# Kernel tuning notes

Hardware: AMD Instinct MI355X
Metric: run time of the kernel (lower is better)

## Reference

```python
import jax, jax.numpy as jnp
from jax import lax
import numpy as np

D_MODEL, D_STATE, EXPAND, D_CONV = 1024, 16, 2, 4
D_INNER = EXPAND * D_MODEL
B, L = 4, 2048


def setup_inputs() -> dict:
    key = jax.random.key(0)
    ks = jax.random.split(key, 12)
    def xavier(k, shape):
        fan_in, fan_out = shape[1], shape[0]
        lim = float(np.sqrt(6.0 / (fan_in + fan_out)))
        return jax.random.uniform(k, shape, jnp.float32, -lim, lim)
    inp = {}
    inp['x'] = jax.random.normal(ks[0], (B, L, D_MODEL), jnp.float32)
    inp['W_left'] = xavier(ks[1], (D_INNER, D_MODEL))
    inp['conv_w'] = jax.random.normal(ks[2], (D_INNER, 1, D_CONV), jnp.float32) * (1.0 / np.sqrt(D_CONV))
    inp['conv_b'] = jax.random.normal(ks[3], (D_INNER,), jnp.float32) * 0.01
    inp['W_delta'] = jax.random.normal(ks[4], (D_INNER, D_INNER), jnp.float32) * (1.0 / np.sqrt(D_INNER))
    inp['b_delta'] = jnp.zeros((D_INNER,), jnp.float32)
    inp['W_B'] = jax.random.normal(ks[5], (D_STATE, D_INNER), jnp.float32) * (1.0 / np.sqrt(D_INNER))
    inp['W_C'] = jax.random.normal(ks[6], (D_STATE, D_INNER), jnp.float32) * (1.0 / np.sqrt(D_INNER))
    inp['A_log'] = jnp.log(jnp.arange(1, D_STATE + 1, dtype=jnp.float32))
    inp['W_right'] = xavier(ks[7], (D_INNER, D_MODEL))
    inp['ln_g'] = jnp.ones((D_INNER,), jnp.float32)
    inp['ln_b'] = jnp.zeros((D_INNER,), jnp.float32)
    inp['W_out'] = xavier(ks[8], (D_MODEL, D_INNER))
    return inp


def _ssm(xl, W_delta, b_delta, W_B, W_C, A_log):
    # xl: [b, l, d_inner]
    b, l, d_inner = xl.shape
    A = -jax.nn.softplus(A_log)  # [d_state]
    delta = jnp.clip(jax.nn.softplus(xl @ W_delta.T + b_delta), 1e-4, 10.0)
    Bm = xl @ W_B.T  # [b, l, d_state]
    Cm = xl @ W_C.T  # [b, l, d_state]

    def step(h, inp):
        d_t, x_t, B_t, C_t = inp  # [b,d_inner], [b,d_inner], [b,N], [b,N]
        A_bar = jnp.exp(d_t[:, :, None] * A)            # [b, d_inner, N]
        h = A_bar * h + (d_t * x_t)[:, :, None] * B_t[:, None, :]
        y_t = jnp.einsum('bdn,bn->bd', h, C_t)
        return h, y_t

    h0 = jnp.zeros((b, d_inner, A_log.shape[0]), xl.dtype)
    xs = (jnp.swapaxes(delta, 0, 1), jnp.swapaxes(xl, 0, 1),
          jnp.swapaxes(Bm, 0, 1), jnp.swapaxes(Cm, 0, 1))
    _, ys = lax.scan(step, h0, xs)  # ys: [l, b, d_inner]
    return jnp.swapaxes(ys, 0, 1)


def reference(x, W_left, conv_w, conv_b, W_delta, b_delta, W_B, W_C, A_log,
              W_right, ln_g, ln_b, W_out):
    d_conv = conv_w.shape[-1]
    # left branch: linear -> causal depthwise conv1d -> silu
    left = x @ W_left.T                          # [b, l, d_inner]
    left_ncw = jnp.swapaxes(left, 1, 2)          # [b, d_inner, l]
    left_ncw = jnp.pad(left_ncw, ((0, 0), (0, 0), (d_conv - 1, 0)))
    left_ncw = lax.conv_general_dilated(
        left_ncw, conv_w, window_strides=(1,), padding='VALID',
        feature_group_count=conv_w.shape[0]) + conv_b[None, :, None]
    left = jax.nn.silu(jnp.swapaxes(left_ncw, 1, 2))
    # selective scan
    ssm_out = _ssm(left, W_delta, b_delta, W_B, W_C, A_log)
    # right gate (eval mode: dropout off)
    gate = jax.nn.silu(x @ W_right.T)
    out = ssm_out * gate
    # layernorm over d_inner
    mu = jnp.mean(out, axis=-1, keepdims=True)
    var = jnp.mean(jnp.square(out - mu), axis=-1, keepdims=True)
    out = (out - mu) * lax.rsqrt(var + 1e-5) * ln_g + ln_b
    return out @ W_out.T
```

## Files before the change

kernel.cpp:

```cpp
#include <hip/hip_runtime.h>
#include <cstddef>

#define LL 2048
#define TOK 8192
#define DM 1024
#define DI 2048
#define NS 16

typedef _Float16 half_t;
typedef __attribute__((ext_vector_type(8))) _Float16 f16x8;
typedef __attribute__((ext_vector_type(4))) _Float16 f16x4;
typedef __attribute__((ext_vector_type(4))) float f32x4;

__device__ __forceinline__ float softplus_f(float x) {
  return fmaxf(x, 0.f) + log1pf(__expf(-fabsf(x)));
}
__device__ __forceinline__ float silu_f(float x) {
  return x / (1.f + __expf(-x));
}
__device__ __forceinline__ void gload_lds16(const void* g, void* l) {
  __builtin_amdgcn_global_load_lds((const __attribute__((address_space(1))) void*)g,
                                   (__attribute__((address_space(3))) void*)l, 16, 0, 0);
}
#define DPP_ADD(v, ctrl) \
  ((v) + __int_as_float(__builtin_amdgcn_update_dpp(0, __float_as_int(v), (ctrl), 0xf, 0xf, true)))

__device__ float g_buf[120881152];

__global__ __launch_bounds__(256) void f2h_k(const float* __restrict__ in,
                                             half_t* __restrict__ out, int n4) {
  const int i = blockIdx.x * 256 + threadIdx.x;
  if (i >= n4) return;
  const float4 v = ((const float4*)in)[i];
  f16x4 o;
  o[0] = (half_t)v.x; o[1] = (half_t)v.y; o[2] = (half_t)v.z; o[3] = (half_t)v.w;
  ((f16x4*)out)[i] = o;
}

__global__ __launch_bounds__(256) void f2h2_k(const float* __restrict__ in,
                                              half_t* __restrict__ hi,
                                              half_t* __restrict__ lo, int n4) {
  const int i = blockIdx.x * 256 + threadIdx.x;
  if (i >= n4) return;
  const float4 v = ((const float4*)in)[i];
  f16x4 h, l;
  h[0] = (half_t)v.x; h[1] = (half_t)v.y; h[2] = (half_t)v.z; h[3] = (half_t)v.w;
  l[0] = (half_t)(v.x - (float)h[0]);
  l[1] = (half_t)(v.y - (float)h[1]);
  l[2] = (half_t)(v.z - (float)h[2]);
  l[3] = (half_t)(v.w - (float)h[3]);
  ((f16x4*)hi)[i] = h;
  ((f16x4*)lo)[i] = l;
}

template <int ACT>
__global__ __launch_bounds__(256) void gemm_mfma(const half_t* __restrict__ A,
                                                 const half_t* __restrict__ W,
                                                 const float* __restrict__ bias,
                                                 float* __restrict__ C,
                                                 int M, int N, int K) {
  __shared__ half_t lA[4096];
  __shared__ half_t lB[4096];
  const int tid = threadIdx.x;
  const int bm0 = blockIdx.y * 128, bn0 = blockIdx.x * 128;
  const int lane = tid & 63, wave = tid >> 6;
  const int q = lane >> 4, mr = lane & 15;
  const int wm = (wave >> 1) * 64, wn = (wave & 1) * 64;
  const int flat0 = tid, flat1 = tid + 256;
  const int kc0 = flat0 >> 7, r0 = flat0 & 127;
  const int kc1 = flat1 >> 7, r1 = flat1 & 127;

  f32x4 acc[4][4];
#pragma unroll
  for (int i = 0; i < 4; ++i)
#pragma unroll
    for (int j = 0; j < 4; ++j) acc[i][j] = (f32x4){0.f, 0.f, 0.f, 0.f};

  for (int k0 = 0; k0 < K; k0 += 32) {
    gload_lds16(A + (size_t)(bm0 + r0) * K + k0 + kc0 * 8, lA + (size_t)flat0 * 8);
    gload_lds16(A + (size_t)(bm0 + r1) * K + k0 + kc1 * 8, lA + (size_t)flat1 * 8);
    gload_lds16(W + (size_t)(bn0 + r0) * K + k0 + kc0 * 8, lB + (size_t)flat0 * 8);
    gload_lds16(W + (size_t)(bn0 + r1) * K + k0 + kc1 * 8, lB + (size_t)flat1 * 8);
    __syncthreads();
    f16x8 af[4], bg[4];
#pragma unroll
    for (int t = 0; t < 4; ++t) {
      af[t] = *(const f16x8*)(lA + ((q << 10) + ((wm + t * 16 + mr) << 3)));
      bg[t] = *(const f16x8*)(lB + ((q << 10) + ((wn + t * 16 + mr) << 3)));
    }
#pragma unroll
    for (int i = 0; i < 4; ++i)
#pragma unroll
      for (int j = 0; j < 4; ++j)
        acc[i][j] = __builtin_amdgcn_mfma_f32_16x16x32_f16(af[i], bg[j], acc[i][j], 0, 0, 0);
    __syncthreads();
  }

#pragma unroll
  for (int i = 0; i < 4; ++i) {
#pragma unroll
    for (int j = 0; j < 4; ++j) {
      const int col = bn0 + wn + j * 16 + mr;
      const float bv = bias ? bias[col] : 0.f;
#pragma unroll
      for (int r = 0; r < 4; ++r) {
        const int row = bm0 + wm + i * 16 + q * 4 + r;
        float v = acc[i][j][r] + bv;
        if (ACT == 1) v = silu_f(v);
        C[(size_t)row * N + col] = v;
      }
    }
  }
}

__global__ __launch_bounds__(256) void gemm_mfma_lg(const half_t* __restrict__ A,
                                                    const half_t* __restrict__ W,
                                                    float* __restrict__ left,
                                                    float* __restrict__ gate) {
  __shared__ half_t lA[4096];
  __shared__ half_t lB[4096];
  const int tid = threadIdx.x;
  const int bm0 = blockIdx.y * 128, bn0 = blockIdx.x * 128;
  const int K = DM;
  const int lane = tid & 63, wave = tid >> 6;
  const int q = lane >> 4, mr = lane & 15;
  const int wm = (wave >> 1) * 64, wn = (wave & 1) * 64;
  const int flat1 = tid + 256;
  const int kc0 = tid >> 7, r0 = tid & 127;
  const int kc1 = flat1 >> 7, r1 = flat1 & 127;

  f32x4 acc[4][4];
#pragma unroll
  for (int i = 0; i < 4; ++i)
#pragma unroll
    for (int j = 0; j < 4; ++j) acc[i][j] = (f32x4){0.f, 0.f, 0.f, 0.f};

  for (int k0 = 0; k0 < K; k0 += 32) {
    gload_lds16(A + (size_t)(bm0 + r0) * K + k0 + kc0 * 8, lA + (size_t)tid * 8);
    gload_lds16(A + (size_t)(bm0 + r1) * K + k0 + kc1 * 8, lA + (size_t)flat1 * 8);
    gload_lds16(W + (size_t)(bn0 + r0) * K + k0 + kc0 * 8, lB + (size_t)tid * 8);
    gload_lds16(W + (size_t)(bn0 + r1) * K + k0 + kc1 * 8, lB + (size_t)flat1 * 8);
    __syncthreads();
    f16x8 af[4], bg[4];
#pragma unroll
    for (int t = 0; t < 4; ++t) {
      af[t] = *(const f16x8*)(lA + ((q << 10) + ((wm + t * 16 + mr) << 3)));
      bg[t] = *(const f16x8*)(lB + ((q << 10) + ((wn + t * 16 + mr) << 3)));
    }
#pragma unroll
    for (int i = 0; i < 4; ++i)
#pragma unroll
      for (int j = 0; j < 4; ++j)
        acc[i][j] = __builtin_amdgcn_mfma_f32_16x16x32_f16(af[i], bg[j], acc[i][j], 0, 0, 0);
    __syncthreads();
  }

  const int is_gate = (bn0 >= DI);
  float* out = is_gate ? gate : left;
  const int cb = bn0 - (is_gate ? DI : 0);
#pragma unroll
  for (int i = 0; i < 4; ++i) {
#pragma unroll
    for (int j = 0; j < 4; ++j) {
      const int col = cb + wn + j * 16 + mr;
#pragma unroll
      for (int r = 0; r < 4; ++r) {
        const int row = bm0 + wm + i * 16 + q * 4 + r;
        float v = acc[i][j][r];
        if (is_gate) v = silu_f(v);
        out[(size_t)row * DI + col] = v;
      }
    }
  }
}

__global__ __launch_bounds__(512, 4) void gemm_mfma_split(const half_t* __restrict__ Ah,
                                                          const half_t* __restrict__ Wh,
                                                          const half_t* __restrict__ Wl,
                                                          const float* __restrict__ bias,
                                                          float* __restrict__ C,
                                                          int M, int N, int K) {
  __shared__ half_t lAh[8192];
  __shared__ half_t lBh[4096], lBl[4096];
  const int tid = threadIdx.x;
  const int bm0 = blockIdx.y * 256, bn0 = blockIdx.x * 128;
  const int lane = tid & 63, wave = tid >> 6;
  const int q = lane >> 4, mr = lane & 15;
  const int wm = (wave >> 1) * 64, wn = (wave & 1) * 64;
  const int aflat1 = tid + 512;
  const int akc0 = tid >> 8, ar0 = tid & 255;
  const int akc1 = aflat1 >> 8, ar1 = aflat1 & 255;
  const int wkc = tid >> 7, wr = tid & 127;

  f32x4 acc[4][4];
#pragma unroll
  for (int i = 0; i < 4; ++i)
#pragma unroll
    for (int j = 0; j < 4; ++j) acc[i][j] = (f32x4){0.f, 0.f, 0.f, 0.f};

  for (int k0 = 0; k0 < K; k0 += 32) {
    gload_lds16(Ah + (size_t)(bm0 + ar0) * K + k0 + akc0 * 8, lAh + (size_t)tid * 8);
    gload_lds16(Ah + (size_t)(bm0 + ar1) * K + k0 + akc1 * 8, lAh + (size_t)aflat1 * 8);
    gload_lds16(Wh + (size_t)(bn0 + wr) * K + k0 + wkc * 8, lBh + (size_t)tid * 8);
    gload_lds16(Wl + (size_t)(bn0 + wr) * K + k0 + wkc * 8, lBl + (size_t)tid * 8);
    __syncthreads();
    f16x8 ah[4], bh[4], bl[4];
#pragma unroll
    for (int t = 0; t < 4; ++t) {
      const int ao = (q << 11) + ((wm + t * 16 + mr) << 3);
      const int bo = (q << 10) + ((wn + t * 16 + mr) << 3);
      ah[t] = *(const f16x8*)(lAh + ao);
      bh[t] = *(const f16x8*)(lBh + bo);
      bl[t] = *(const f16x8*)(lBl + bo);
    }
#pragma unroll
    for (int i = 0; i < 4; ++i)
#pragma unroll
      for (int j = 0; j < 4; ++j) {
        acc[i][j] = __builtin_amdgcn_mfma_f32_16x16x32_f16(ah[i], bh[j], acc[i][j], 0, 0, 0);
        acc[i][j] = __builtin_amdgcn_mfma_f32_16x16x32_f16(ah[i], bl[j], acc[i][j], 0, 0, 0);
      }
    __syncthreads();
  }

  const int wmg = (wave >> 1) * 64;
#pragma unroll
  for (int i = 0; i < 4; ++i) {
#pragma unroll
    for (int j = 0; j < 4; ++j) {
      const int col = bn0 + wn + j * 16 + mr;
      const float bv = bias[col];
#pragma unroll
      for (int r = 0; r < 4; ++r) {
        const int row = bm0 + wmg + i * 16 + q * 4 + r;
        float v = softplus_f(acc[i][j][r] + bv);
        v = fminf(fmaxf(v, 1e-4f), 10.f);
        C[(size_t)row * N + col] = v;
      }
    }
  }
}

__global__ __launch_bounds__(256) void bc_mfma(const half_t* __restrict__ A,
                                               const half_t* __restrict__ Wbc,
                                               float* __restrict__ bc) {
  __shared__ half_t lA[4096];
  __shared__ half_t lB[1024];
  const int tid = threadIdx.x;
  const int bm0 = blockIdx.x * 128;
  const int lane = tid & 63, wave = tid >> 6;
  const int q = lane >> 4, mr = lane & 15;
  const int wm = wave * 32;
  const int flat1 = tid + 256;
  const int kcA0 = tid >> 7, rA0 = tid & 127;
  const int kcA1 = flat1 >> 7, rA1 = flat1 & 127;
  const int kcB = tid >> 5, rB = tid & 31;

  f32x4 acc[2][2];
#pragma unroll
  for (int i = 0; i < 2; ++i)
#pragma unroll
    for (int j = 0; j < 2; ++j) acc[i][j] = (f32x4){0.f, 0.f, 0.f, 0.f};

  for (int k0 = 0; k0 < DI; k0 += 32) {
    gload_lds16(A + (size_t)(bm0 + rA0) * DI + k0 + kcA0 * 8, lA + (size_t)tid * 8);
    gload_lds16(A + (size_t)(bm0 + rA1) * DI + k0 + kcA1 * 8, lA + (size_t)flat1 * 8);
    if (tid < 128)
      gload_lds16(Wbc + (size_t)rB * DI + k0 + kcB * 8, lB + (size_t)tid * 8);
    __syncthreads();
    f16x8 af[2], bg[2];
#pragma unroll
    for (int t = 0; t < 2; ++t) {
      af[t] = *(const f16x8*)(lA + ((q << 10) + ((wm + t * 16 + mr) << 3)));
      bg[t] = *(const f16x8*)(lB + ((q << 8) + ((t * 16 + mr) << 3)));
    }
#pragma unroll
    for (int i = 0; i < 2; ++i)
#pragma unroll
      for (int j = 0; j < 2; ++j)
        acc[i][j] = __builtin_amdgcn_mfma_f32_16x16x32_f16(af[i], bg[j], acc[i][j], 0, 0, 0);
    __syncthreads();
  }

#pragma unroll
  for (int i = 0; i < 2; ++i) {
#pragma unroll
    for (int j = 0; j < 2; ++j) {
#pragma unroll
      for (int r = 0; r < 4; ++r) {
        const int row = bm0 + wm + i * 16 + q * 4 + r;
        bc[(size_t)row * 32 + 2 * mr + j] = acc[i][j][r];
      }
    }
  }
}

__global__ __launch_bounds__(256) void conv_silu_k(const float* __restrict__ left,
                                                   const float* __restrict__ cw,
                                                   const float* __restrict__ cb,
                                                   float* __restrict__ xc,
                                                   half_t* __restrict__ xch) {
  const int idx = blockIdx.x * 256 + threadIdx.x;
  const int d = idx & (DI - 1);
  const int bt = idx >> 11;
  const int t = bt & (LL - 1);
  const float4 wv = *(const float4*)(cw + (size_t)d * 4);
  float acc = cb[d];
  const size_t base = (size_t)idx;
  if (t >= 3) {
    acc += left[base - 3 * DI] * wv.x + left[base - 2 * DI] * wv.y +
           left[base - DI] * wv.z + left[base] * wv.w;
  } else {
    acc += left[base] * wv.w;
    if (t >= 1) acc += left[base - DI] * wv.z;
    if (t >= 2) acc += left[base - 2 * DI] * wv.y;
  }
  const float v = silu_f(acc);
  xc[base] = v;
  xch[base] = (half_t)v;
}

#define ST 32
__global__ __launch_bounds__(256) void scan_k(const float* __restrict__ delta,
                                              const float* __restrict__ xc,
                                              const float* __restrict__ gate,
                                              const float* __restrict__ bcp,
                                              const float* __restrict__ A_log,
                                              float* __restrict__ y) {
  __shared__ float dx2[16 * 68];
  __shared__ float bcs[ST * 32];
  __shared__ float ys[ST * 16];
  const int tid = threadIdx.x;
  const int b  = blockIdx.x >> 7;
  const int d0 = (blockIdx.x & 127) << 4;
  const int n  = tid & 15;
  const int ch = tid >> 4;
  const float An = -softplus_f(A_log[n]);

  const int t_a = tid >> 4, c_a = tid & 15;
  const int t_b = t_a + 16;

  float h = 0.f;
  const size_t batch_base = (size_t)b * LL * DI + d0;
  const size_t batch_bc   = (size_t)b * LL * 32;

  size_t rb_cur = batch_base;
  float g0, g1;
  {
    const size_t ra = rb_cur + (size_t)t_a * DI + c_a;
    const size_t rbx = rb_cur + (size_t)t_b * DI + c_a;
    const float d0v = delta[ra], x0v = xc[ra];
    const float d1v = delta[rbx], x1v = xc[rbx];
    g0 = gate[ra]; g1 = gate[rbx];
    const float2 b0 = *(const float2*)&bcp[batch_bc + (size_t)t_a * 32 + 2 * c_a];
    const float2 b1 = *(const float2*)&bcp[batch_bc + (size_t)t_b * 32 + 2 * c_a];
    *(float2*)&dx2[c_a * 68 + t_a * 2] = make_float2(d0v, x0v);
    *(float2*)&dx2[c_a * 68 + t_b * 2] = make_float2(d1v, x1v);
    *(float2*)&bcs[t_a * 32 + 2 * c_a] = b0;
    *(float2*)&bcs[t_b * 32 + 2 * c_a] = b1;
  }
  __syncthreads();

  for (int it = 0; it < LL / ST; ++it) {
    float nd0, nx0, ng0, nd1, nx1, ng1;
    float2 nb0, nb1;
    const size_t rb_nxt = batch_base + (size_t)(it + 1) * ST * DI;
    if (it + 1 < LL / ST) {
      const size_t ra = rb_nxt + (size_t)t_a * DI + c_a;
      const size_t rbx = rb_nxt + (size_t)t_b * DI + c_a;
      nd0 = delta[ra]; nx0 = xc[ra]; ng0 = gate[ra];
      nd1 = delta[rbx]; nx1 = xc[rbx]; ng1 = gate[rbx];
      const size_t bcb = batch_bc + (size_t)(it + 1) * ST * 32;
      nb0 = *(const float2*)&bcp[bcb + (size_t)t_a * 32 + 2 * c_a];
      nb1 = *(const float2*)&bcp[bcb + (size_t)t_b * 32 + 2 * c_a];
    }

    const float* dxp = &dx2[ch * 68];
#pragma unroll
    for (int tt = 0; tt < ST; tt += 2) {
      const float4 v = *(const float4*)&dxp[tt * 2];
      const float2 bc0 = *(const float2*)&bcs[tt * 32 + 2 * n];
      const float2 bc1 = *(const float2*)&bcs[(tt + 1) * 32 + 2 * n];
      float ab = __expf(v.x * An);
      h = fmaf(ab, h, v.x * v.y * bc0.x);
      float p = h * bc0.y;
      p = DPP_ADD(p, 0x111); p = DPP_ADD(p, 0x112);
      p = DPP_ADD(p, 0x114); p = DPP_ADD(p, 0x118);
      if (n == 15) ys[tt * 16 + ch] = p;
      ab = __expf(v.z * An);
      h = fmaf(ab, h, v.z * v.w * bc1.x);
      p = h * bc1.y;
      p = DPP_ADD(p, 0x111); p = DPP_ADD(p, 0x112);
      p = DPP_ADD(p, 0x114); p = DPP_ADD(p, 0x118);
      if (n == 15) ys[(tt + 1) * 16 + ch] = p;
    }
    __syncthreads();

    if (it + 1 < LL / ST) {
      *(float2*)&dx2[c_a * 68 + t_a * 2] = make_float2(nd0, nx0);
      *(float2*)&dx2[c_a * 68 + t_b * 2] = make_float2(nd1, nx1);
      *(float2*)&bcs[t_a * 32 + 2 * c_a] = nb0;
      *(float2*)&bcs[t_b * 32 + 2 * c_a] = nb1;
    }
    y[rb_cur + (size_t)t_a * DI + c_a] = ys[t_a * 16 + c_a] * g0;
    y[rb_cur + (size_t)t_b * DI + c_a] = ys[t_b * 16 + c_a] * g1;
    g0 = ng0; g1 = ng1;
    rb_cur = rb_nxt;
    __syncthreads();
  }
}

__global__ __launch_bounds__(256) void ln_k(const float* __restrict__ y,
                                            const float* __restrict__ gam,
                                            const float* __restrict__ bet,
                                            half_t* __restrict__ outn) {
  const int row = blockIdx.x;
  const int tid = threadIdx.x;
  const float* yr = y + (size_t)row * DI;
  const float4 v0 = ((const float4*)yr)[tid];
  const float4 v1 = ((const float4*)yr)[tid + 256];
  float s = v0.x + v0.y + v0.z + v0.w + v1.x + v1.y + v1.z + v1.w;
  float q = v0.x * v0.x + v0.y * v0.y + v0.z * v0.z + v0.w * v0.w +
            v1.x * v1.x + v1.y * v1.y + v1.z * v1.z + v1.w * v1.w;
  for (int off = 32; off > 0; off >>= 1) {
    s += __shfl_down(s, off);
    q += __shfl_down(q, off);
  }
  __shared__ float sred[4], qred[4];
  const int wid = tid >> 6;
  if ((tid & 63) == 0) { sred[wid] = s; qred[wid] = q; }
  __syncthreads();
  s = sred[0] + sred[1] + sred[2] + sred[3];
  q = qred[0] + qred[1] + qred[2] + qred[3];
  const float mu = s * (1.f / DI);
  const float rs = rsqrtf(q * (1.f / DI) - mu * mu + 1e-5f);
  half_t* orow = outn + (size_t)row * DI;
  const int c0 = tid * 4, c1 = (tid + 256) * 4;
  f16x4 o;
  o[0] = (half_t)((v0.x - mu) * rs * gam[c0 + 0] + bet[c0 + 0]);
  o[1] = (half_t)((v0.y - mu) * rs * gam[c0 + 1] + bet[c0 + 1]);
  o[2] = (half_t)((v0.z - mu) * rs * gam[c0 + 2] + bet[c0 + 2]);
  o[3] = (half_t)((v0.w - mu) * rs * gam[c0 + 3] + bet[c0 + 3]);
  ((f16x4*)orow)[tid] = o;
  o[0] = (half_t)((v1.x - mu) * rs * gam[c1 + 0] + bet[c1 + 0]);
  o[1] = (half_t)((v1.y - mu) * rs * gam[c1 + 1] + bet[c1 + 1]);
  o[2] = (half_t)((v1.z - mu) * rs * gam[c1 + 2] + bet[c1 + 2]);
  o[3] = (half_t)((v1.w - mu) * rs * gam[c1 + 3] + bet[c1 + 3]);
  ((f16x4*)orow)[tid + 256] = o;
}

extern "C" void kernel_launch(void* const* d_in, const int* in_sizes, int n_in,
                              void* d_out, int out_size, void* d_ws, size_t ws_size,
                              hipStream_t stream) {
  const float* x       = (const float*)d_in[0];
  const float* W_left  = (const float*)d_in[1];
  const float* conv_w  = (const float*)d_in[2];
  const float* conv_b  = (const float*)d_in[3];
  const float* W_delta = (const float*)d_in[4];
  const float* b_delta = (const float*)d_in[5];
  const float* W_B     = (const float*)d_in[6];
  const float* W_C     = (const float*)d_in[7];
  const float* A_log   = (const float*)d_in[8];
  const float* W_right = (const float*)d_in[9];
  const float* ln_g    = (const float*)d_in[10];
  const float* ln_b    = (const float*)d_in[11];
  const float* W_out   = (const float*)d_in[12];

  float* buf = nullptr;
  hipGetSymbolAddress((void**)&buf, HIP_SYMBOL(g_buf));
  half_t* xh   = (half_t*)(buf + 0);
  half_t* wlgh = (half_t*)(buf + 4194304);
  half_t* wrh  = (half_t*)(buf + 5242880);
  half_t* wdh  = (half_t*)(buf + 6291456);
  half_t* wdl  = (half_t*)(buf + 8388608);
  half_t* woh  = (half_t*)(buf + 10485760);
  float* left  = buf + 11534336;
  float* xc    = buf + 28311552;
  half_t* xch  = (half_t*)(buf + 45088768);
  float* dlt   = buf + 61865984;
  float* gate  = buf + 78643200;
  float* yv    = buf + 95420416;
  half_t* nrmh = (half_t*)(buf + 112197632);
  float* bc    = buf + 120586240;
  half_t* wbch = (half_t*)(buf + 120848384);

  f2h_k<<<8192, 256, 0, stream>>>(x, xh, TOK * DM / 4);
  f2h_k<<<2048, 256, 0, stream>>>(W_left, wlgh, DI * DM / 4);
  f2h_k<<<2048, 256, 0, stream>>>(W_right, wrh, DI * DM / 4);
  f2h_k<<<2048, 256, 0, stream>>>(W_out, woh, DM * DI / 4);
  f2h2_k<<<4096, 256, 0, stream>>>(W_delta, wdh, wdl, DI * DI / 4);
  f2h_k<<<32, 256, 0, stream>>>(W_B, wbch, NS * DI / 4);
  f2h_k<<<32, 256, 0, stream>>>(W_C, wbch + NS * DI, NS * DI / 4);

  gemm_mfma_lg<<<dim3(2 * DI / 128, TOK / 128), 256, 0, stream>>>(xh, wlgh, left, gate);
  conv_silu_k<<<TOK * DI / 256, 256, 0, stream>>>(left, conv_w, conv_b, xc, xch);
  gemm_mfma_split<<<dim3(DI / 128, TOK / 256), 512, 0, stream>>>(xch, wdh, wdl, b_delta, dlt, TOK, DI, DI);
  bc_mfma<<<TOK / 128, 256, 0, stream>>>(xch, wbch, bc);
  scan_k<<<512, 256, 0, stream>>>(dlt, xc, gate, bc, A_log, yv);
  ln_k<<<TOK, 256, 0, stream>>>(yv, ln_g, ln_b, nrmh);
  gemm_mfma<0><<<dim3(DM / 128, TOK / 128), 256, 0, stream>>>(nrmh, woh, nullptr, (float*)d_out, TOK, DM, DI);
}
```

Before: 930.4 us.

## Replace split-precision delta GEMM with pipelined 256x256 single-fp16 MFMA kernel

Drops the hi/lo fp16 split of W_delta, which halves the MFMA work and the weight traffic of the delta projection. The delta GEMM becomes a 256x256-tile, 8-wave kernel with K-step 64. Global-to-LDS loads are double-buffered and interleaved into four quadrant phases, with explicit vmcnt waits and s_setprio around the MFMA bursts. The trade is lower precision in delta, since the W_delta rounding error is no longer compensated, and heavy 128KB LDS use that limits occupancy.

```diff
diff --git a/kernel.cpp b/kernel.cpp
--- a/kernel.cpp
+++ b/kernel.cpp
@@ -35,22 +35,6 @@
   f16x4 o;
   o[0] = (half_t)v.x; o[1] = (half_t)v.y; o[2] = (half_t)v.z; o[3] = (half_t)v.w;
   ((f16x4*)out)[i] = o;
-}
-
-__global__ __launch_bounds__(256) void f2h2_k(const float* __restrict__ in,
-                                              half_t* __restrict__ hi,
-                                              half_t* __restrict__ lo, int n4) {
-  const int i = blockIdx.x * 256 + threadIdx.x;
-  if (i >= n4) return;
-  const float4 v = ((const float4*)in)[i];
-  f16x4 h, l;
-  h[0] = (half_t)v.x; h[1] = (half_t)v.y; h[2] = (half_t)v.z; h[3] = (half_t)v.w;
-  l[0] = (half_t)(v.x - (float)h[0]);
-  l[1] = (half_t)(v.y - (float)h[1]);
-  l[2] = (half_t)(v.z - (float)h[2]);
-  l[3] = (half_t)(v.w - (float)h[3]);
-  ((f16x4*)hi)[i] = h;
-  ((f16x4*)lo)[i] = l;
 }
 
 template <int ACT>
@@ -174,68 +158,119 @@
   }
 }
 
-__global__ __launch_bounds__(512, 4) void gemm_mfma_split(const half_t* __restrict__ Ah,
-                                                          const half_t* __restrict__ Wh,
-                                                          const half_t* __restrict__ Wl,
-                                                          const float* __restrict__ bias,
-                                                          float* __restrict__ C,
-                                                          int M, int N, int K) {
-  __shared__ half_t lAh[8192];
-  __shared__ half_t lBh[4096], lBl[4096];
+#define STAGE_A8(tt, h)                                                         \
+  do {                                                                          \
+    const size_t gb = (size_t)(bm0 + (h) * 128) * DI + (size_t)(tt) * 64;       \
+    half_t* lb = lds8 + ((((tt) & 1) * 2 + (h)) * 8192);                        \
+    gload_lds16(A + gb + (size_t)srow0 * DI + skc0 * 8, lb + sf0 * 8);          \
+    gload_lds16(A + gb + (size_t)srow1 * DI + skc1 * 8, lb + sf1 * 8);          \
+  } while (0)
+#define STAGE_B8(tt, g)                                                         \
+  do {                                                                          \
+    const size_t gb = (size_t)(bn0 + (g) * 128) * DI + (size_t)(tt) * 64;       \
+    half_t* lb = lds8 + (32768 + (((tt) & 1) * 2 + (g)) * 8192);                \
+    gload_lds16(W + gb + (size_t)srow0 * DI + skc0 * 8, lb + sf0 * 8);          \
+    gload_lds16(W + gb + (size_t)srow1 * DI + skc1 * 8, lb + sf1 * 8);          \
+  } while (0)
+#define ACC8(qd, mi, nj) acc[(qd) & 1][mi][(qd) >> 1][nj]
+#define PHASE8(tt, qd, STG, WN)                                                 \
+  do {                                                                          \
+    asm volatile("s_waitcnt vmcnt(" #WN ")" ::: "memory");                      \
+    __builtin_amdgcn_s_barrier();                                               \
+    STG;                                                                        \
+    const half_t* Ab = lds8 + ((((tt) & 1) * 2 + ((qd) & 1)) * 8192);           \
+    const half_t* Bb = lds8 + (32768 + (((tt) & 1) * 2 + ((qd) >> 1)) * 8192);  \
+    f16x8 af0[4], af1[4], bf0[2], bf1[2];                                       \
+    _Pragma("unroll")                                                           \
+    for (int mi = 0; mi < 4; ++mi) {                                            \
+      af0[mi] = *(const f16x8*)(Ab + ((q * 128 + wsm + mi * 16 + mr) << 3));    \
+      af1[mi] = *(const f16x8*)(Ab + (((q + 4) * 128 + wsm + mi * 16 + mr) << 3)); \
+    }                                                                           \
+    _Pragma("unroll")                                                           \
+    for (int nj = 0; nj < 2; ++nj) {                                            \
+      bf0[nj] = *(const f16x8*)(Bb + ((q * 128 + wsn + nj * 16 + mr) << 3));    \
+      bf1[nj] = *(const f16x8*)(Bb + (((q + 4) * 128 + wsn + nj * 16 + mr) << 3)); \
+    }                                                                           \
+    __builtin_amdgcn_s_setprio(1);                                              \
+    _Pragma("unroll")                                                           \
+    for (int mi = 0; mi < 4; ++mi)                                              \
+      _Pragma("unroll")                                                         \
+      for (int nj = 0; nj < 2; ++nj) {                                          \
+        ACC8(qd, mi, nj) = __builtin_amdgcn_mfma_f32_16x16x32_f16(af0[mi], bf0[nj], ACC8(qd, mi, nj), 0, 0, 0); \
+        ACC8(qd, mi, nj) = __builtin_amdgcn_mfma_f32_16x16x32_f16(af1[mi], bf1[nj], ACC8(qd, mi, nj), 0, 0, 0); \
+      }                                                                         \
+    __builtin_amdgcn_s_setprio(0);                                              \
+  } while (0)
+
+__global__ __launch_bounds__(512, 2) void gemm_delta8(const half_t* __restrict__ A,
+                                                      const half_t* __restrict__ W,
+                                                      const float* __restrict__ bias,
+                                                      float* __restrict__ dlt) {
+  __shared__ half_t lds8[65536];
   const int tid = threadIdx.x;
-  const int bm0 = blockIdx.y * 256, bn0 = blockIdx.x * 128;
+  const int bm0 = blockIdx.y * 256, bn0 = blockIdx.x * 256;
   const int lane = tid & 63, wave = tid >> 6;
   const int q = lane >> 4, mr = lane & 15;
-  const int wm = (wave >> 1) * 64, wn = (wave & 1) * 64;
-  const int aflat1 = tid + 512;
-  const int akc0 = tid >> 8, ar0 = tid & 255;
-  const int akc1 = aflat1 >> 8, ar1 = aflat1 & 255;
-  const int wkc = tid >> 7, wr = tid & 127;
-
-  f32x4 acc[4][4];
-#pragma unroll
-  for (int i = 0; i < 4; ++i)
-#pragma unroll
-    for (int j = 0; j < 4; ++j) acc[i][j] = (f32x4){0.f, 0.f, 0.f, 0.f};
-
-  for (int k0 = 0; k0 < K; k0 += 32) {
-    gload_lds16(Ah + (size_t)(bm0 + ar0) * K + k0 + akc0 * 8, lAh + (size_t)tid * 8);
-    gload_lds16(Ah + (size_t)(bm0 + ar1) * K + k0 + akc1 * 8, lAh + (size_t)aflat1 * 8);
-    gload_lds16(Wh + (size_t)(bn0 + wr) * K + k0 + wkc * 8, lBh + (size_t)tid * 8);
-    gload_lds16(Wl + (size_t)(bn0 + wr) * K + k0 + wkc * 8, lBl + (size_t)tid * 8);
-    __syncthreads();
-    f16x8 ah[4], bh[4], bl[4];
-#pragma unroll
-    for (int t = 0; t < 4; ++t) {
-      const int ao = (q << 11) + ((wm + t * 16 + mr) << 3);
-      const int bo = (q << 10) + ((wn + t * 16 + mr) << 3);
-      ah[t] = *(const f16x8*)(lAh + ao);
-      bh[t] = *(const f16x8*)(lBh + bo);
-      bl[t] = *(const f16x8*)(lBl + bo);
-    }
-#pragma unroll
-    for (int i = 0; i < 4; ++i)
-#pragma unroll
-      for (int j = 0; j < 4; ++j) {
-        acc[i][j] = __builtin_amdgcn_mfma_f32_16x16x32_f16(ah[i], bh[j], acc[i][j], 0, 0, 0);
-        acc[i][j] = __builtin_amdgcn_mfma_f32_16x16x32_f16(ah[i], bl[j], acc[i][j], 0, 0, 0);
-      }
-    __syncthreads();
-  }
-
-  const int wmg = (wave >> 1) * 64;
-#pragma unroll
-  for (int i = 0; i < 4; ++i) {
-#pragma unroll
-    for (int j = 0; j < 4; ++j) {
-      const int col = bn0 + wn + j * 16 + mr;
-      const float bv = bias[col];
-#pragma unroll
-      for (int r = 0; r < 4; ++r) {
-        const int row = bm0 + wmg + i * 16 + q * 4 + r;
-        float v = softplus_f(acc[i][j][r] + bv);
-        v = fminf(fmaxf(v, 1e-4f), 10.f);
-        C[(size_t)row * N + col] = v;
+  const int wsm = (wave >> 2) * 64;
+  const int wsn = (wave & 3) * 32;
+  const int sf0 = tid, sf1 = tid + 512;
+  const int skc0 = sf0 >> 7, srow0 = sf0 & 127;
+  const int skc1 = sf1 >> 7, srow1 = sf1 & 127;
+
+  f32x4 acc[2][4][2][2];
+#pragma unroll
+  for (int h = 0; h < 2; ++h)
+#pragma unroll
+    for (int mi = 0; mi < 4; ++mi)
+#pragma unroll
+      for (int g = 0; g < 2; ++g)
+#pragma unroll
+        for (int nj = 0; nj < 2; ++nj) acc[h][mi][g][nj] = (f32x4){0.f, 0.f, 0.f, 0.f};
+
+  STAGE_A8(0, 0);
+  STAGE_B8(0, 0);
+  STAGE_A8(0, 1);
+  STAGE_B8(0, 1);
+  STAGE_A8(1, 0);
+
+  for (int it = 0; it < 15; ++it) {
+    const int t0 = 2 * it, t1 = 2 * it + 1;
+    PHASE8(t0, 0, STAGE_B8(t0 + 1, 0), 6);
+    PHASE8(t0, 1, STAGE_A8(t0 + 1, 1), 6);
+    PHASE8(t0, 2, STAGE_B8(t0 + 1, 1), 6);
+    PHASE8(t0, 3, STAGE_A8(t0 + 2, 0), 6);
+    PHASE8(t1, 0, STAGE_B8(t1 + 1, 0), 6);
+    PHASE8(t1, 1, STAGE_A8(t1 + 1, 1), 6);
+    PHASE8(t1, 2, STAGE_B8(t1 + 1, 1), 6);
+    PHASE8(t1, 3, STAGE_A8(t1 + 2, 0), 6);
+  }
+  PHASE8(30, 0, STAGE_B8(31, 0), 6);
+  PHASE8(30, 1, STAGE_A8(31, 1), 6);
+  PHASE8(30, 2, STAGE_B8(31, 1), 6);
+  PHASE8(30, 3, (void)0, 6);
+  PHASE8(31, 0, (void)0, 4);
+  PHASE8(31, 1, (void)0, 2);
+  PHASE8(31, 2, (void)0, 0);
+  PHASE8(31, 3, (void)0, 0);
+
+#pragma unroll
+  for (int h = 0; h < 2; ++h) {
+#pragma unroll
+    for (int mi = 0; mi < 4; ++mi) {
+#pragma unroll
+      for (int g = 0; g < 2; ++g) {
+#pragma unroll
+        for (int nj = 0; nj < 2; ++nj) {
+          const int col = bn0 + g * 128 + wsn + nj * 16 + mr;
+          const float bv = bias[col];
+#pragma unroll
+          for (int r = 0; r < 4; ++r) {
+            const int row = bm0 + h * 128 + wsm + mi * 16 + q * 4 + r;
+            float v = softplus_f(acc[h][mi][g][nj][r] + bv);
+            v = fminf(fmaxf(v, 1e-4f), 10.f);
+            dlt[(size_t)row * DI + col] = v;
+          }
+        }
       }
     }
   }
@@ -472,7 +507,6 @@
   half_t* wlgh = (half_t*)(buf + 4194304);
   half_t* wrh  = (half_t*)(buf + 5242880);
   half_t* wdh  = (half_t*)(buf + 6291456);
-  half_t* wdl  = (half_t*)(buf + 8388608);
   half_t* woh  = (half_t*)(buf + 10485760);
   float* left  = buf + 11534336;
   float* xc    = buf + 28311552;
@@ -488,13 +522,13 @@
   f2h_k<<<2048, 256, 0, stream>>>(W_left, wlgh, DI * DM / 4);
   f2h_k<<<2048, 256, 0, stream>>>(W_right, wrh, DI * DM / 4);
   f2h_k<<<2048, 256, 0, stream>>>(W_out, woh, DM * DI / 4);
-  f2h2_k<<<4096, 256, 0, stream>>>(W_delta, wdh, wdl, DI * DI / 4);
+  f2h_k<<<4096, 256, 0, stream>>>(W_delta, wdh, DI * DI / 4);
   f2h_k<<<32, 256, 0, stream>>>(W_B, wbch, NS * DI / 4);
   f2h_k<<<32, 256, 0, stream>>>(W_C, wbch + NS * DI, NS * DI / 4);
 
   gemm_mfma_lg<<<dim3(2 * DI / 128, TOK / 128), 256, 0, stream>>>(xh, wlgh, left, gate);
   conv_silu_k<<<TOK * DI / 256, 256, 0, stream>>>(left, conv_w, conv_b, xc, xch);
-  gemm_mfma_split<<<dim3(DI / 128, TOK / 256), 512, 0, stream>>>(xch, wdh, wdl, b_delta, dlt, TOK, DI, DI);
+  gemm_delta8<<<dim3(DI / 256, TOK / 256), 512, 0, stream>>>(xch, wdh, b_delta, dlt);
   bc_mfma<<<TOK / 128, 256, 0, stream>>>(xch, wbch, bc);
   scan_k<<<512, 256, 0, stream>>>(dlt, xc, gate, bc, A_log, yv);
   ln_k<<<TOK, 256, 0, stream>>>(yv, ln_g, ln_b, nrmh);
```

Result: slower. 980.9 us (+5.4%).

## Split-K the delta, BC and output GEMMs and drop the W_delta lo-part

Applied to the files above, without the earlier changes.

The delta GEMM drops the hi/lo split of W_delta and runs a single f16 MFMA pass split over K in two halves, with a separate finalize kernel that adds the partials, bias, softplus and clamp. The B/C projection is split 8-way over K and the output GEMM 4-way, each followed by a reduction kernel, which gives these small-grid GEMMs more blocks to fill the GPU. Partials are written into scratch buffers that are reused. This adds extra partial-sum memory traffic and more launches, and dropping the lo correction lowers the precision of delta.

```diff
diff --git a/kernel.cpp b/kernel.cpp
--- a/kernel.cpp
+++ b/kernel.cpp
@@ -35,82 +35,6 @@
   f16x4 o;
   o[0] = (half_t)v.x; o[1] = (half_t)v.y; o[2] = (half_t)v.z; o[3] = (half_t)v.w;
   ((f16x4*)out)[i] = o;
-}
-
-__global__ __launch_bounds__(256) void f2h2_k(const float* __restrict__ in,
-                                              half_t* __restrict__ hi,
-                                              half_t* __restrict__ lo, int n4) {
-  const int i = blockIdx.x * 256 + threadIdx.x;
-  if (i >= n4) return;
-  const float4 v = ((const float4*)in)[i];
-  f16x4 h, l;
-  h[0] = (half_t)v.x; h[1] = (half_t)v.y; h[2] = (half_t)v.z; h[3] = (half_t)v.w;
-  l[0] = (half_t)(v.x - (float)h[0]);
-  l[1] = (half_t)(v.y - (float)h[1]);
-  l[2] = (half_t)(v.z - (float)h[2]);
-  l[3] = (half_t)(v.w - (float)h[3]);
-  ((f16x4*)hi)[i] = h;
-  ((f16x4*)lo)[i] = l;
-}
-
-template <int ACT>
-__global__ __launch_bounds__(256) void gemm_mfma(const half_t* __restrict__ A,
-                                                 const half_t* __restrict__ W,
-                                                 const float* __restrict__ bias,
-                                                 float* __restrict__ C,
-                                                 int M, int N, int K) {
-  __shared__ half_t lA[4096];
-  __shared__ half_t lB[4096];
-  const int tid = threadIdx.x;
-  const int bm0 = blockIdx.y * 128, bn0 = blockIdx.x * 128;
-  const int lane = tid & 63, wave = tid >> 6;
-  const int q = lane >> 4, mr = lane & 15;
-  const int wm = (wave >> 1) * 64, wn = (wave & 1) * 64;
-  const int flat0 = tid, flat1 = tid + 256;
-  const int kc0 = flat0 >> 7, r0 = flat0 & 127;
-  const int kc1 = flat1 >> 7, r1 = flat1 & 127;
-
-  f32x4 acc[4][4];
-#pragma unroll
-  for (int i = 0; i < 4; ++i)
-#pragma unroll
-    for (int j = 0; j < 4; ++j) acc[i][j] = (f32x4){0.f, 0.f, 0.f, 0.f};
-
-  for (int k0 = 0; k0 < K; k0 += 32) {
-    gload_lds16(A + (size_t)(bm0 + r0) * K + k0 + kc0 * 8, lA + (size_t)flat0 * 8);
-    gload_lds16(A + (size_t)(bm0 + r1) * K + k0 + kc1 * 8, lA + (size_t)flat1 * 8);
-    gload_lds16(W + (size_t)(bn0 + r0) * K + k0 + kc0 * 8, lB + (size_t)flat0 * 8);
-    gload_lds16(W + (size_t)(bn0 + r1) * K + k0 + kc1 * 8, lB + (size_t)flat1 * 8);
-    __syncthreads();
-    f16x8 af[4], bg[4];
-#pragma unroll
-    for (int t = 0; t < 4; ++t) {
-      af[t] = *(const f16x8*)(lA + ((q << 10) + ((wm + t * 16 + mr) << 3)));
-      bg[t] = *(const f16x8*)(lB + ((q << 10) + ((wn + t * 16 + mr) << 3)));
-    }
-#pragma unroll
-    for (int i = 0; i < 4; ++i)
-#pragma unroll
-      for (int j = 0; j < 4; ++j)
-        acc[i][j] = __builtin_amdgcn_mfma_f32_16x16x32_f16(af[i], bg[j], acc[i][j], 0, 0, 0);
-    __syncthreads();
-  }
-
-#pragma unroll
-  for (int i = 0; i < 4; ++i) {
-#pragma unroll
-    for (int j = 0; j < 4; ++j) {
-      const int col = bn0 + wn + j * 16 + mr;
-      const float bv = bias ? bias[col] : 0.f;
-#pragma unroll
-      for (int r = 0; r < 4; ++r) {
-        const int row = bm0 + wm + i * 16 + q * 4 + r;
-        float v = acc[i][j][r] + bv;
-        if (ACT == 1) v = silu_f(v);
-        C[(size_t)row * N + col] = v;
-      }
-    }
-  }
 }
 
 __global__ __launch_bounds__(256) void gemm_mfma_lg(const half_t* __restrict__ A,
@@ -174,16 +98,16 @@
   }
 }
 
-__global__ __launch_bounds__(512, 4) void gemm_mfma_split(const half_t* __restrict__ Ah,
-                                                          const half_t* __restrict__ Wh,
-                                                          const half_t* __restrict__ Wl,
-                                                          const float* __restrict__ bias,
-                                                          float* __restrict__ C,
-                                                          int M, int N, int K) {
-  __shared__ half_t lAh[8192];
-  __shared__ half_t lBh[4096], lBl[4096];
+__global__ __launch_bounds__(512, 8) void gemm_delta_sk(const half_t* __restrict__ A,
+                                                        const half_t* __restrict__ W,
+                                                        float* __restrict__ P0,
+                                                        float* __restrict__ P1) {
+  __shared__ half_t lA[8192];
+  __shared__ half_t lB[4096];
   const int tid = threadIdx.x;
   const int bm0 = blockIdx.y * 256, bn0 = blockIdx.x * 128;
+  const int K = DI;
+  const int kz = blockIdx.z * (DI / 2);
   const int lane = tid & 63, wave = tid >> 6;
   const int q = lane >> 4, mr = lane & 15;
   const int wm = (wave >> 1) * 64, wn = (wave & 1) * 64;
@@ -198,56 +122,69 @@
 #pragma unroll
     for (int j = 0; j < 4; ++j) acc[i][j] = (f32x4){0.f, 0.f, 0.f, 0.f};
 
-  for (int k0 = 0; k0 < K; k0 += 32) {
-    gload_lds16(Ah + (size_t)(bm0 + ar0) * K + k0 + akc0 * 8, lAh + (size_t)tid * 8);
-    gload_lds16(Ah + (size_t)(bm0 + ar1) * K + k0 + akc1 * 8, lAh + (size_t)aflat1 * 8);
-    gload_lds16(Wh + (size_t)(bn0 + wr) * K + k0 + wkc * 8, lBh + (size_t)tid * 8);
-    gload_lds16(Wl + (size_t)(bn0 + wr) * K + k0 + wkc * 8, lBl + (size_t)tid * 8);
-    __syncthreads();
-    f16x8 ah[4], bh[4], bl[4];
+  for (int k0 = kz; k0 < kz + DI / 2; k0 += 32) {
+    gload_lds16(A + (size_t)(bm0 + ar0) * K + k0 + akc0 * 8, lA + (size_t)tid * 8);
+    gload_lds16(A + (size_t)(bm0 + ar1) * K + k0 + akc1 * 8, lA + (size_t)aflat1 * 8);
+    gload_lds16(W + (size_t)(bn0 + wr) * K + k0 + wkc * 8, lB + (size_t)tid * 8);
+    __syncthreads();
+    f16x8 ah[4], bg[4];
 #pragma unroll
     for (int t = 0; t < 4; ++t) {
       const int ao = (q << 11) + ((wm + t * 16 + mr) << 3);
       const int bo = (q << 10) + ((wn + t * 16 + mr) << 3);
-      ah[t] = *(const f16x8*)(lAh + ao);
-      bh[t] = *(const f16x8*)(lBh + bo);
-      bl[t] = *(const f16x8*)(lBl + bo);
-    }
+      ah[t] = *(const f16x8*)(lA + ao);
+      bg[t] = *(const f16x8*)(lB + bo);
+    }
+    __builtin_amdgcn_s_setprio(1);
 #pragma unroll
     for (int i = 0; i < 4; ++i)
 #pragma unroll
-      for (int j = 0; j < 4; ++j) {
-        acc[i][j] = __builtin_amdgcn_mfma_f32_16x16x32_f16(ah[i], bh[j], acc[i][j], 0, 0, 0);
-        acc[i][j] = __builtin_amdgcn_mfma_f32_16x16x32_f16(ah[i], bl[j], acc[i][j], 0, 0, 0);
-      }
-    __syncthreads();
-  }
-
-  const int wmg = (wave >> 1) * 64;
+      for (int j = 0; j < 4; ++j)
+        acc[i][j] = __builtin_amdgcn_mfma_f32_16x16x32_f16(ah[i], bg[j], acc[i][j], 0, 0, 0);
+    __builtin_amdgcn_s_setprio(0);
+    __syncthreads();
+  }
+
+  float* P = blockIdx.z ? P1 : P0;
 #pragma unroll
   for (int i = 0; i < 4; ++i) {
 #pragma unroll
     for (int j = 0; j < 4; ++j) {
       const int col = bn0 + wn + j * 16 + mr;
-      const float bv = bias[col];
 #pragma unroll
       for (int r = 0; r < 4; ++r) {
-        const int row = bm0 + wmg + i * 16 + q * 4 + r;
-        float v = softplus_f(acc[i][j][r] + bv);
-        v = fminf(fmaxf(v, 1e-4f), 10.f);
-        C[(size_t)row * N + col] = v;
+        const int row = bm0 + wm + i * 16 + q * 4 + r;
+        P[(size_t)row * DI + col] = acc[i][j][r];
       }
     }
   }
 }
 
-__global__ __launch_bounds__(256) void bc_mfma(const half_t* __restrict__ A,
-                                               const half_t* __restrict__ Wbc,
-                                               float* __restrict__ bc) {
+__global__ __launch_bounds__(256) void delta_fin(const float* __restrict__ P0,
+                                                 const float* __restrict__ P1,
+                                                 const float* __restrict__ bias,
+                                                 float* __restrict__ dlt) {
+  const int i = blockIdx.x * 256 + threadIdx.x;
+  const float4 a = ((const float4*)P0)[i];
+  const float4 b = ((const float4*)P1)[i];
+  const int col4 = (i * 4) & (DI - 1);
+  const float4 bv = *(const float4*)&bias[col4];
+  float4 o;
+  o.x = fminf(fmaxf(softplus_f(a.x + b.x + bv.x), 1e-4f), 10.f);
+  o.y = fminf(fmaxf(softplus_f(a.y + b.y + bv.y), 1e-4f), 10.f);
+  o.z = fminf(fmaxf(softplus_f(a.z + b.z + bv.z), 1e-4f), 10.f);
+  o.w = fminf(fmaxf(softplus_f(a.w + b.w + bv.w), 1e-4f), 10.f);
+  ((float4*)dlt)[i] = o;
+}
+
+__global__ __launch_bounds__(256, 8) void bc_sk(const half_t* __restrict__ A,
+                                                const half_t* __restrict__ Wbc,
+                                                float* __restrict__ bcP) {
   __shared__ half_t lA[4096];
   __shared__ half_t lB[1024];
   const int tid = threadIdx.x;
   const int bm0 = blockIdx.x * 128;
+  const int kz = blockIdx.y * (DI / 8);
   const int lane = tid & 63, wave = tid >> 6;
   const int q = lane >> 4, mr = lane & 15;
   const int wm = wave * 32;
@@ -262,7 +199,7 @@
 #pragma unroll
     for (int j = 0; j < 2; ++j) acc[i][j] = (f32x4){0.f, 0.f, 0.f, 0.f};
 
-  for (int k0 = 0; k0 < DI; k0 += 32) {
+  for (int k0 = kz; k0 < kz + DI / 8; k0 += 32) {
     gload_lds16(A + (size_t)(bm0 + rA0) * DI + k0 + kcA0 * 8, lA + (size_t)tid * 8);
     gload_lds16(A + (size_t)(bm0 + rA1) * DI + k0 + kcA1 * 8, lA + (size_t)flat1 * 8);
     if (tid < 128)
@@ -282,6 +219,7 @@
     __syncthreads();
   }
 
+  float* P = bcP + (size_t)blockIdx.y * (TOK * 32);
 #pragma unroll
   for (int i = 0; i < 2; ++i) {
 #pragma unroll
@@ -289,10 +227,94 @@
 #pragma unroll
       for (int r = 0; r < 4; ++r) {
         const int row = bm0 + wm + i * 16 + q * 4 + r;
-        bc[(size_t)row * 32 + 2 * mr + j] = acc[i][j][r];
+        P[(size_t)row * 32 + 2 * mr + j] = acc[i][j][r];
       }
     }
   }
+}
+
+__global__ __launch_bounds__(256) void bc_fin(const float* __restrict__ bcP,
+                                              float* __restrict__ bc) {
+  const int i = blockIdx.x * 256 + threadIdx.x;
+  float4 s = ((const float4*)bcP)[i];
+#pragma unroll
+  for (int z = 1; z < 8; ++z) {
+    const float4 v = ((const float4*)(bcP + (size_t)z * (TOK * 32)))[i];
+    s.x += v.x; s.y += v.y; s.z += v.z; s.w += v.w;
+  }
+  ((float4*)bc)[i] = s;
+}
+
+__global__ __launch_bounds__(256, 8) void gemm_out_sk(const half_t* __restrict__ A,
+                                                      const half_t* __restrict__ W,
+                                                      float* __restrict__ Pout) {
+  __shared__ half_t lA[4096];
+  __shared__ half_t lB[4096];
+  const int tid = threadIdx.x;
+  const int bm0 = blockIdx.y * 128, bn0 = blockIdx.x * 128;
+  const int K = DI, N = DM;
+  const int kz = blockIdx.z * (DI / 4);
+  const int lane = tid & 63, wave = tid >> 6;
+  const int q = lane >> 4, mr = lane & 15;
+  const int wm = (wave >> 1) * 64, wn = (wave & 1) * 64;
+  const int flat1 = tid + 256;
+  const int kc0 = tid >> 7, r0 = tid & 127;
+  const int kc1 = flat1 >> 7, r1 = flat1 & 127;
+
+  f32x4 acc[4][4];
+#pragma unroll
+  for (int i = 0; i < 4; ++i)
+#pragma unroll
+    for (int j = 0; j < 4; ++j) acc[i][j] = (f32x4){0.f, 0.f, 0.f, 0.f};
+
+  for (int k0 = kz; k0 < kz + DI / 4; k0 += 32) {
+    gload_lds16(A + (size_t)(bm0 + r0) * K + k0 + kc0 * 8, lA + (size_t)tid * 8);
+    gload_lds16(A + (size_t)(bm0 + r1) * K + k0 + kc1 * 8, lA + (size_t)flat1 * 8);
+    gload_lds16(W + (size_t)(bn0 + r0) * K + k0 + kc0 * 8, lB + (size_t)tid * 8);
+    gload_lds16(W + (size_t)(bn0 + r1) * K + k0 + kc1 * 8, lB + (size_t)flat1 * 8);
+    __syncthreads();
+    f16x8 af[4], bg[4];
+#pragma unroll
+    for (int t = 0; t < 4; ++t) {
+      af[t] = *(const f16x8*)(lA + ((q << 10) + ((wm + t * 16 + mr) << 3)));
+      bg[t] = *(const f16x8*)(lB + ((q << 10) + ((wn + t * 16 + mr) << 3)));
+    }
+#pragma unroll
+    for (int i = 0; i < 4; ++i)
+#pragma unroll
+      for (int j = 0; j < 4; ++j)
+        acc[i][j] = __builtin_amdgcn_mfma_f32_16x16x32_f16(af[i], bg[j], acc[i][j], 0, 0, 0);
+    __syncthreads();
+  }
+
+  float* P = Pout + (size_t)blockIdx.z * (TOK * DM);
+#pragma unroll
+  for (int i = 0; i < 4; ++i) {
+#pragma unroll
+    for (int j = 0; j < 4; ++j) {
+      const int col = bn0 + wn + j * 16 + mr;
+#pragma unroll
+      for (int r = 0; r < 4; ++r) {
+        const int row = bm0 + wm + i * 16 + q * 4 + r;
+        P[(size_t)row * N + col] = acc[i][j][r];
+      }
+    }
+  }
+}
+
+__global__ __launch_bounds__(256) void out_fin(const float* __restrict__ Pout,
+                                               float* __restrict__ C) {
+  const int i = blockIdx.x * 256 + threadIdx.x;
+  const float4 a = ((const float4*)Pout)[i];
+  const float4 b = ((const float4*)(Pout + (size_t)TOK * DM))[i];
+  const float4 c = ((const float4*)(Pout + (size_t)2 * TOK * DM))[i];
+  const float4 d = ((const float4*)(Pout + (size_t)3 * TOK * DM))[i];
+  float4 o;
+  o.x = a.x + b.x + c.x + d.x;
+  o.y = a.y + b.y + c.y + d.y;
+  o.z = a.z + b.z + c.z + d.z;
+  o.w = a.w + b.w + c.w + d.w;
+  ((float4*)C)[i] = o;
 }
 
 __global__ __launch_bounds__(256) void conv_silu_k(const float* __restrict__ left,
@@ -472,7 +494,6 @@
   half_t* wlgh = (half_t*)(buf + 4194304);
   half_t* wrh  = (half_t*)(buf + 5242880);
   half_t* wdh  = (half_t*)(buf + 6291456);
-  half_t* wdl  = (half_t*)(buf + 8388608);
   half_t* woh  = (half_t*)(buf + 10485760);
   float* left  = buf + 11534336;
   float* xc    = buf + 28311552;
@@ -483,20 +504,27 @@
   half_t* nrmh = (half_t*)(buf + 112197632);
   float* bc    = buf + 120586240;
   half_t* wbch = (half_t*)(buf + 120848384);
+  float* dP0   = left;
+  float* dP1   = yv;
+  float* bcP   = buf + 0;
+  float* outP  = left;
 
   f2h_k<<<8192, 256, 0, stream>>>(x, xh, TOK * DM / 4);
   f2h_k<<<2048, 256, 0, stream>>>(W_left, wlgh, DI * DM / 4);
   f2h_k<<<2048, 256, 0, stream>>>(W_right, wrh, DI * DM / 4);
   f2h_k<<<2048, 256, 0, stream>>>(W_out, woh, DM * DI / 4);
-  f2h2_k<<<4096, 256, 0, stream>>>(W_delta, wdh, wdl, DI * DI / 4);
+  f2h_k<<<4096, 256, 0, stream>>>(W_delta, wdh, DI * DI / 4);
   f2h_k<<<32, 256, 0, stream>>>(W_B, wbch, NS * DI / 4);
   f2h_k<<<32, 256, 0, stream>>>(W_C, wbch + NS * DI, NS * DI / 4);
 
   gemm_mfma_lg<<<dim3(2 * DI / 128, TOK / 128), 256, 0, stream>>>(xh, wlgh, left, gate);
   conv_silu_k<<<TOK * DI / 256, 256, 0, stream>>>(left, conv_w, conv_b, xc, xch);
-  gemm_mfma_split<<<dim3(DI / 128, TOK / 256), 512, 0, stream>>>(xch, wdh, wdl, b_delta, dlt, TOK, DI, DI);
-  bc_mfma<<<TOK / 128, 256, 0, stream>>>(xch, wbch, bc);
+  gemm_delta_sk<<<dim3(DI / 128, TOK / 256, 2), 512, 0, stream>>>(xch, wdh, dP0, dP1);
+  delta_fin<<<TOK * DI / 1024, 256, 0, stream>>>(dP0, dP1, b_delta, dlt);
+  bc_sk<<<dim3(TOK / 128, 8), 256, 0, stream>>>(xch, wbch, bcP);
+  bc_fin<<<TOK * 32 / 1024, 256, 0, stream>>>(bcP, bc);
   scan_k<<<512, 256, 0, stream>>>(dlt, xc, gate, bc, A_log, yv);
   ln_k<<<TOK, 256, 0, stream>>>(yv, ln_g, ln_b, nrmh);
-  gemm_mfma<0><<<dim3(DM / 128, TOK / 128), 256, 0, stream>>>(nrmh, woh, nullptr, (float*)d_out, TOK, DM, DI);
-}
+  gemm_out_sk<<<dim3(DM / 128, TOK / 128, 4), 256, 0, stream>>>(nrmh, woh, outP);
+  out_fin<<<TOK * DM / 1024, 256, 0, stream>>>(outP, (float*)d_out);
+}
```

New measurement: 2.479 ms. 2.66x slower.
